# Kernel optimization log

Hardware: AMD Instinct MI355X
Metric: run time of the kernel (lower is better)

## Reference

```python
import jax, jax.numpy as jnp
import numpy as np

B = 32; H = 56; W = 56; C = 384; WS = 7; SHIFT = 3; NH = 12; HID = 1536; RANK = 192
N = WS * WS
NWIN = (H // WS) * (W // WS)


def _rel_index():
    coords = np.stack(np.meshgrid(np.arange(WS), np.arange(WS), indexing='ij')).reshape(2, -1)
    rel = (coords[:, :, None] - coords[:, None, :]).transpose(1, 2, 0)
    rel[..., 0] += WS - 1
    rel[..., 1] += WS - 1
    rel[..., 0] *= 2 * WS - 1
    return jnp.asarray(rel.sum(-1).reshape(-1))  # (N*N,) int


def _attn_mask():
    img = np.zeros((H, W))
    cnt = 0
    sls = (slice(0, -WS), slice(-WS, -SHIFT), slice(-SHIFT, None))
    for hs in sls:
        for ws_ in sls:
            img[hs, ws_] = cnt
            cnt += 1
    mw = img.reshape(H // WS, WS, W // WS, WS).transpose(0, 2, 1, 3).reshape(-1, N)
    am = mw[:, None, :] - mw[:, :, None]
    return jnp.asarray(np.where(am != 0, -100.0, 0.0).astype(np.float32))  # (nW,N,N)


REL_IDX = _rel_index()
ATTN_MASK = _attn_mask()


def _ln(x, g, b):
    m = x.mean(-1, keepdims=True)
    v = ((x - m) ** 2).mean(-1, keepdims=True)
    return (x - m) / jnp.sqrt(v + 1e-5) * g + b


def _flin(x, v, u, b):
    # FactorizedLinear: x @ V^T @ U^T + b
    return (x @ v.T) @ u.T + b


def setup_inputs() -> dict:
    key = jax.random.key(0)
    ks = jax.random.split(key, 12)
    def n(k, shape, s):
        return jax.random.normal(k, shape, jnp.float32) * s
    return {
        'x': jax.random.normal(ks[0], (B, H * W, C), jnp.float32),
        'norm1_g': jnp.ones((C,), jnp.float32), 'norm1_b': jnp.zeros((C,), jnp.float32),
        'rpb_table': n(ks[1], ((2 * WS - 1) ** 2, NH), 0.02),
        'qkv_v': n(ks[2], (RANK, C), 0.05), 'qkv_u': n(ks[3], (3 * C, RANK), 0.05),
        'qkv_b': jnp.zeros((3 * C,), jnp.float32),
        'proj_v': n(ks[4], (RANK, C), 0.05), 'proj_u': n(ks[5], (C, RANK), 0.05),
        'proj_b': jnp.zeros((C,), jnp.float32),
        'norm2_g': jnp.ones((C,), jnp.float32), 'norm2_b': jnp.zeros((C,), jnp.float32),
        'fc1_v': n(ks[6], (RANK, C), 0.05), 'fc1_u': n(ks[7], (HID, RANK), 0.05),
        'fc1_b': jnp.zeros((HID,), jnp.float32),
        'fc2_v': n(ks[8], (RANK, HID), 0.05), 'fc2_u': n(ks[9], (C, RANK), 0.05),
        'fc2_b': jnp.zeros((C,), jnp.float32),
    }


def reference(x, norm1_g, norm1_b, rpb_table, qkv_v, qkv_u, qkv_b,
              proj_v, proj_u, proj_b, norm2_g, norm2_b,
              fc1_v, fc1_u, fc1_b, fc2_v, fc2_u, fc2_b):
    hd = C // NH
    scale = hd ** -0.5
    shortcut = x
    y = _ln(x, norm1_g, norm1_b).reshape(B, H, W, C)
    y = jnp.roll(y, (-SHIFT, -SHIFT), axis=(1, 2))  # cyclic shift
    # window partition -> (B*nW, N, C)
    y = y.reshape(B, H // WS, WS, W // WS, WS, C).transpose(0, 1, 3, 2, 4, 5).reshape(-1, N, C)
    qkv = _flin(y, qkv_v, qkv_u, qkv_b).reshape(-1, N, 3, NH, hd).transpose(2, 0, 3, 1, 4)
    q, k, v = qkv[0] * scale, qkv[1], qkv[2]  # (B*nW, NH, N, hd)
    attn = jnp.einsum('bhnd,bhmd->bhnm', q, k)
    rpb = rpb_table[REL_IDX].reshape(N, N, NH).transpose(2, 0, 1)  # (NH,N,N)
    attn = attn + rpb[None]
    attn = attn.reshape(B, NWIN, NH, N, N) + ATTN_MASK[None, :, None]
    attn = jax.nn.softmax(attn, axis=-1).reshape(-1, NH, N, N)
    o = jnp.einsum('bhnm,bhmd->bhnd', attn, v).transpose(0, 2, 1, 3).reshape(-1, N, C)
    o = _flin(o, proj_v, proj_u, proj_b)
    # window reverse + reverse shift
    o = o.reshape(B, H // WS, W // WS, WS, WS, C).transpose(0, 1, 3, 2, 4, 5).reshape(B, H, W, C)
    o = jnp.roll(o, (SHIFT, SHIFT), axis=(1, 2)).reshape(B, H * W, C)
    x = shortcut + o
    z = _ln(x, norm2_g, norm2_b)
    z = jax.nn.gelu(_flin(z, fc1_v, fc1_u, fc1_b), approximate=False)
    z = _flin(z, fc2_v, fc2_u, fc2_b)
    return x + z
```

## Files before the change

### kernel.cpp

```cpp
#include <hip/hip_runtime.h>
#include <hip/hip_bf16.h>

using bf16 = __hip_bfloat16;
typedef __bf16 bf16x8 __attribute__((ext_vector_type(8)));
typedef __bf16 bf16x4v __attribute__((ext_vector_type(4)));
typedef float f32x4 __attribute__((ext_vector_type(4)));

#define MROWS 100352

__device__ __forceinline__ void async16(void* l, const void* g) {
    void* gg = const_cast<void*>(g);
    __builtin_amdgcn_global_load_lds((__attribute__((address_space(1))) void*)gg,
                                     (__attribute__((address_space(3))) void*)l, 16, 0, 0);
}

__device__ __forceinline__ float gelu_f(float x) {
    float u = x * fmaf(0.044715f * x, x, 1.0f);
    float e = __expf(-1.5957691216057308f * u);
    return x * __builtin_amdgcn_rcpf(1.0f + e);
}

struct Cvt8 { const float* s[8]; bf16* d[8]; int n[8]; };

__global__ __launch_bounds__(256) void cvt8_k(Cvt8 c) {
    int seg = blockIdx.y;
    int i4 = (blockIdx.x * 256 + threadIdx.x) * 4;
    if (i4 < c.n[seg]) {
        float4 v = *(const float4*)(c.s[seg] + i4);
        bf16* d = c.d[seg] + i4;
        d[0] = __float2bfloat16(v.x);
        d[1] = __float2bfloat16(v.y);
        d[2] = __float2bfloat16(v.z);
        d[3] = __float2bfloat16(v.w);
    }
}

__global__ __launch_bounds__(384) void wmerge_k(const float* __restrict__ u,
                                                const float* __restrict__ v,
                                                bf16* __restrict__ wm) {
    int o = blockIdx.x, i = threadIdx.x;
    const float* ur = u + o * 192;
    float acc = 0.f;
    for (int r = 0; r < 192; ++r) acc = fmaf(ur[r], v[r * 384 + i], acc);
    wm[o * 384 + i] = __float2bfloat16(acc);
}

__global__ __launch_bounds__(256) void bias_pre_k(const float* __restrict__ rpbt,
                                                  float* __restrict__ biasf) {
    int wt = blockIdx.x / 12, h = blockIdx.x % 12;
    int t = threadIdx.x;
    int lane = t >> 2, tb = t & 3;
    int hi = lane >> 4, lo = lane & 15;
    int m = tb * 16 + lo;
    bool bH = (wt & 2) != 0, bW = (wt & 1) != 0;
    float* outb = biasf + (size_t)blockIdx.x * 4096;
    int mm = m < 49 ? m : 0;
    int i2 = mm / 7, j2 = mm % 7;
    int rm = (bH ? (i2 < 4 ? 1 : 2) : 0) * 3 + (bW ? (j2 < 4 ? 1 : 2) : 0);
#pragma unroll
    for (int ta = 0; ta < 4; ++ta) {
#pragma unroll
        for (int j = 0; j < 4; ++j) {
            int n = ta * 16 + hi * 4 + j;
            float v;
            if (n < 49 && m < 49) {
                int i1 = n / 7, j1 = n % 7;
                int rn = (bH ? (i1 < 4 ? 1 : 2) : 0) * 3 + (bW ? (j1 < 4 ? 1 : 2) : 0);
                v = rpbt[((i1 - i2 + 6) * 13 + (j1 - j2 + 6)) * 12 + h];
                if (rn != rm) v -= 100.0f;
            } else {
                v = -1e30f;
            }
            outb[(ta * 4 + j) * 256 + t] = v;
        }
    }
}

__global__ __launch_bounds__(256) void ln1_window_k(const float* __restrict__ x,
                                                    const float* __restrict__ g,
                                                    const float* __restrict__ bta,
                                                    bf16* __restrict__ ywin) {
    int wrow = blockIdx.x * 4 + (threadIdx.x >> 6);
    int lane = threadIdx.x & 63;
    int tok = wrow % 49, win = wrow / 49;
    int i = tok / 7, j = tok % 7;
    int wwi = win & 7, whi = (win >> 3) & 7, bi = win >> 6;
    int hs = (whi * 7 + i + 3) % 56;
    int ws_ = (wwi * 7 + j + 3) % 56;
    const float* xr = x + ((size_t)bi * 3136 + (size_t)hs * 56 + ws_) * 384;
    float v[6]; float s = 0.f, s2 = 0.f;
#pragma unroll
    for (int u = 0; u < 6; ++u) { float t = xr[lane + 64 * u]; v[u] = t; s += t; s2 += t * t; }
#pragma unroll
    for (int d = 1; d < 64; d <<= 1) { s += __shfl_xor(s, d); s2 += __shfl_xor(s2, d); }
    float mean = s * (1.0f / 384.0f);
    float var = s2 * (1.0f / 384.0f) - mean * mean;
    float rstd = rsqrtf(var + 1e-5f);
    bf16* yr = ywin + (size_t)wrow * 384;
#pragma unroll
    for (int u = 0; u < 6; ++u) {
        int c = lane + 64 * u;
        yr[c] = __float2bfloat16((v[u] - mean) * rstd * g[c] + bta[c]);
    }
}

__global__ __launch_bounds__(256) void resid_ln2_k(const float* __restrict__ x,
                                                   const bf16* __restrict__ proj,
                                                   const float* __restrict__ g,
                                                   const float* __restrict__ bta,
                                                   float* __restrict__ x2,
                                                   bf16* __restrict__ z) {
    int row = blockIdx.x * 4 + (threadIdx.x >> 6);
    int lane = threadIdx.x & 63;
    int bi = row / 3136; int hw = row % 3136;
    int h = hw / 56, w = hw % 56;
    int h2 = (h + 53) % 56, w2 = (w + 53) % 56;
    int prow = ((bi * 8 + h2 / 7) * 8 + w2 / 7) * 49 + (h2 % 7) * 7 + (w2 % 7);
    const float* xr = x + (size_t)row * 384;
    const bf16* pr = proj + (size_t)prow * 384;
    float* x2r = x2 + (size_t)row * 384;
    float v[6]; float s = 0.f, s2 = 0.f;
#pragma unroll
    for (int u = 0; u < 6; ++u) {
        int c = lane + 64 * u;
        float t = xr[c] + __bfloat162float(pr[c]);
        v[u] = t; s += t; s2 += t * t;
        x2r[c] = t;
    }
#pragma unroll
    for (int d = 1; d < 64; d <<= 1) { s += __shfl_xor(s, d); s2 += __shfl_xor(s2, d); }
    float mean = s * (1.0f / 384.0f);
    float var = s2 * (1.0f / 384.0f) - mean * mean;
    float rstd = rsqrtf(var + 1e-5f);
    bf16* zr = z + (size_t)row * 384;
#pragma unroll
    for (int u = 0; u < 6; ++u) {
        int c = lane + 64 * u;
        zr[c] = __float2bfloat16((v[u] - mean) * rstd * g[c] + bta[c]);
    }
}

__global__ __launch_bounds__(256) void attn_mfma_k(const bf16* __restrict__ qkv,
                                                   const float* __restrict__ biasf,
                                                   bf16* __restrict__ o) {
    __shared__ __align__(16) __bf16 vt_s[4][32 * 72];
    __shared__ __align__(16) __bf16 p_s[4][32 * 72];
    const int win = blockIdx.x;
    const int r = blockIdx.y;
    const int wave = threadIdx.x >> 6, lane = threadIdx.x & 63;
    const int lo = lane & 15, hi = lane >> 4;
    const int whi = (win >> 3) & 7, wwi = win & 7;
    const int wt = ((whi == 7) ? 2 : 0) + ((wwi == 7) ? 1 : 0);
    __bf16* vt_w = vt_s[wave];
    __bf16* p_w = p_s[wave];
    const int h = r * 4 + wave;
    const bf16* qbase = qkv + (size_t)win * 49 * 1152 + h * 32;
    const float* btile = biasf + (size_t)(wt * 12 + h) * 4096;
    bf16x8 zf = {};

    {
        int m = lane;
        bf16x8 vrow[4];
#pragma unroll
        for (int d8 = 0; d8 < 4; ++d8)
            vrow[d8] = (m < 49) ? *(const bf16x8*)(qbase + (size_t)m * 1152 + 768 + d8 * 8) : zf;
#pragma unroll
        for (int d8 = 0; d8 < 4; ++d8)
#pragma unroll
            for (int e = 0; e < 8; ++e)
                vt_w[(d8 * 8 + e) * 72 + m] = vrow[d8][e];
    }
    bf16x8 aq[4], bk[4];
    const int kq = hi * 8;
#pragma unroll
    for (int ta = 0; ta < 4; ++ta) {
        int n = ta * 16 + lo;
        aq[ta] = (n < 49) ? *(const bf16x8*)(qbase + (size_t)n * 1152 + kq) : zf;
        bk[ta] = (n < 49) ? *(const bf16x8*)(qbase + (size_t)n * 1152 + 384 + kq) : zf;
    }
    f32x4 acc[4][4] = {};
#pragma unroll
    for (int ta = 0; ta < 4; ++ta)
#pragma unroll
        for (int tb = 0; tb < 4; ++tb)
            acc[ta][tb] = __builtin_amdgcn_mfma_f32_16x16x32_bf16(aq[ta], bk[tb], acc[ta][tb], 0, 0, 0);
#pragma unroll
    for (int ta = 0; ta < 4; ++ta) {
#pragma unroll
        for (int j = 0; j < 4; ++j) {
            float4 b4 = *(const float4*)(btile + (ta * 4 + j) * 256 + lane * 4);
            acc[ta][0][j] = fmaf(acc[ta][0][j], 0.17677669529663687f, b4.x);
            acc[ta][1][j] = fmaf(acc[ta][1][j], 0.17677669529663687f, b4.y);
            acc[ta][2][j] = fmaf(acc[ta][2][j], 0.17677669529663687f, b4.z);
            acc[ta][3][j] = fmaf(acc[ta][3][j], 0.17677669529663687f, b4.w);
        }
    }
    bf16x8 vb[2][2];
#pragma unroll
    for (int kb = 0; kb < 2; ++kb)
#pragma unroll
        for (int tb = 0; tb < 2; ++tb)
            vb[kb][tb] = *(const bf16x8*)(vt_w + (tb * 16 + lo) * 72 + kb * 32 + hi * 8);

    f32x4 oacc[4][2] = {};
#pragma unroll
    for (int half = 0; half < 2; ++half) {
#pragma unroll
        for (int tq = 0; tq < 2; ++tq) {
            int ta = half * 2 + tq;
#pragma unroll
            for (int j = 0; j < 4; ++j) {
                float mx = fmaxf(fmaxf(acc[ta][0][j], acc[ta][1][j]),
                                 fmaxf(acc[ta][2][j], acc[ta][3][j]));
                mx = fmaxf(mx, __shfl_xor(mx, 1));
                mx = fmaxf(mx, __shfl_xor(mx, 2));
                mx = fmaxf(mx, __shfl_xor(mx, 4));
                mx = fmaxf(mx, __shfl_xor(mx, 8));
                float e0 = __expf(acc[ta][0][j] - mx);
                float e1 = __expf(acc[ta][1][j] - mx);
                float e2 = __expf(acc[ta][2][j] - mx);
                float e3 = __expf(acc[ta][3][j] - mx);
                float sm = e0 + e1 + e2 + e3;
                sm += __shfl_xor(sm, 1);
                sm += __shfl_xor(sm, 2);
                sm += __shfl_xor(sm, 4);
                sm += __shfl_xor(sm, 8);
                float inv = __builtin_amdgcn_rcpf(sm);
                int nl = tq * 16 + hi * 4 + j;
                p_w[nl * 72 + lo]      = (__bf16)(e0 * inv);
                p_w[nl * 72 + 16 + lo] = (__bf16)(e1 * inv);
                p_w[nl * 72 + 32 + lo] = (__bf16)(e2 * inv);
                p_w[nl * 72 + 48 + lo] = (__bf16)(e3 * inv);
            }
        }
#pragma unroll
        for (int kb = 0; kb < 2; ++kb) {
#pragma unroll
            for (int tq = 0; tq < 2; ++tq) {
                bf16x8 pa = *(const bf16x8*)(p_w + (tq * 16 + lo) * 72 + kb * 32 + hi * 8);
#pragma unroll
                for (int tb = 0; tb < 2; ++tb)
                    oacc[half * 2 + tq][tb] =
                        __builtin_amdgcn_mfma_f32_16x16x32_bf16(pa, vb[kb][tb], oacc[half * 2 + tq][tb], 0, 0, 0);
            }
        }
    }
    bf16* obase = o + (size_t)win * 49 * 384 + h * 32;
#pragma unroll
    for (int ta = 0; ta < 4; ++ta) {
#pragma unroll
        for (int j = 0; j < 4; ++j) {
            int n = ta * 16 + hi * 4 + j;
            if (n < 49) {
#pragma unroll
                for (int tb = 0; tb < 2; ++tb)
                    obase[(size_t)n * 384 + tb * 16 + lo] = __float2bfloat16(oacc[ta][tb][j]);
            }
        }
    }
}

template <int K, int N, int WN, int EPI>
__global__ __launch_bounds__(WN * 128, 8 - WN) void gemm_bt(const bf16* __restrict__ A,
                                                            const bf16* __restrict__ W,
                                                            const float* __restrict__ bias,
                                                            void* __restrict__ Cout) {
    constexpr int T = WN * 128;
    constexpr int BN = WN * 32;
    __shared__ __align__(16) bf16 lds_a[128 * 64];
    __shared__ __align__(16) bf16 lds_b[BN * 64];
    const int t = threadIdx.x;
    const int wave = t >> 6, lane = t & 63;
    const int gdx = gridDim.x;
    int flat = blockIdx.y * gdx + blockIdx.x;
    int q = (gdx * gridDim.y) >> 3;
    int work = (flat & 7) * q + (flat >> 3);
    const int n0 = (work % gdx) * BN, m0 = (work / gdx) * 128;
    const int wm = wave / WN, wn = wave % WN;
    const int fr = lane & 15, hi = lane >> 4;
    const int srow = t >> 3;
    const int gslot = (t & 7) ^ (srow & 7);
    const bf16* abase = A + (size_t)(m0 + srow) * K + gslot * 8;
    const bf16* bbase = W + (size_t)(n0 + srow) * K + gslot * 8;
    char* la = (char*)lds_a + t * 16;
    char* lb = (char*)lds_b + t * 16;
    const int fp = fr & 7;
    const char* ra0 = (const char*)lds_a + (wm * 64 + fr) * 128 + (hi ^ fp) * 16;
    const char* ra1 = (const char*)lds_a + (wm * 64 + fr) * 128 + ((4 + hi) ^ fp) * 16;
    const char* rb0 = (const char*)lds_b + (wn * 32 + fr) * 128 + (hi ^ fp) * 16;
    const char* rb1 = (const char*)lds_b + (wn * 32 + fr) * 128 + ((4 + hi) ^ fp) * 16;
    f32x4 acc[4][2] = {};
#pragma unroll
    for (int kt = 0; kt < K; kt += 64) {
        if (kt > 0) __syncthreads();
#pragma unroll
        for (int i = 0; i < 1024 / T; ++i)
            async16(la + i * T * 16, abase + (size_t)i * (T >> 3) * K + kt);
#pragma unroll
        for (int i = 0; i < BN * 8 / T; ++i)
            async16(lb + i * T * 16, bbase + (size_t)i * (T >> 3) * K + kt);
        __syncthreads();
        bf16x8 af[4], bfr[2];
#pragma unroll
        for (int mi = 0; mi < 4; ++mi) af[mi] = *(const bf16x8*)(ra0 + mi * 2048);
#pragma unroll
        for (int ni = 0; ni < 2; ++ni) bfr[ni] = *(const bf16x8*)(rb0 + ni * 2048);
#pragma unroll
        for (int mi = 0; mi < 4; ++mi)
#pragma unroll
            for (int ni = 0; ni < 2; ++ni)
                acc[mi][ni] = __builtin_amdgcn_mfma_f32_16x16x32_bf16(bfr[ni], af[mi], acc[mi][ni], 0, 0, 0);
#pragma unroll
        for (int mi = 0; mi < 4; ++mi) af[mi] = *(const bf16x8*)(ra1 + mi * 2048);
#pragma unroll
        for (int ni = 0; ni < 2; ++ni) bfr[ni] = *(const bf16x8*)(rb1 + ni * 2048);
#pragma unroll
        for (int mi = 0; mi < 4; ++mi)
#pragma unroll
            for (int ni = 0; ni < 2; ++ni)
                acc[mi][ni] = __builtin_amdgcn_mfma_f32_16x16x32_bf16(bfr[ni], af[mi], acc[mi][ni], 0, 0, 0);
    }
    const int rq4 = hi * 4;
    const int ncol = n0 + wn * 32 + rq4;
    const size_t cbase = (size_t)(m0 + wm * 64 + fr) * N + ncol;
    const float* pb = bias ? bias + ncol : nullptr;
#pragma unroll
    for (int mi = 0; mi < 4; ++mi) {
#pragma unroll
        for (int ni = 0; ni < 2; ++ni) {
            float v0 = acc[mi][ni][0], v1 = acc[mi][ni][1];
            float v2 = acc[mi][ni][2], v3 = acc[mi][ni][3];
            if (pb) {
                float4 b4 = *(const float4*)(pb + ni * 16);
                v0 += b4.x; v1 += b4.y; v2 += b4.z; v3 += b4.w;
            }
            if (EPI == 1) { v0 = gelu_f(v0); v1 = gelu_f(v1); v2 = gelu_f(v2); v3 = gelu_f(v3); }
            if (EPI == 2) {
                float4* p = (float4*)((float*)Cout + cbase + (size_t)mi * 16 * N + ni * 16);
                float4 o = *p;
                o.x += v0; o.y += v1; o.z += v2; o.w += v3;
                *p = o;
            } else {
                bf16x4v st = { (__bf16)v0, (__bf16)v1, (__bf16)v2, (__bf16)v3 };
                *(bf16x4v*)((bf16*)Cout + cbase + (size_t)mi * 16 * N + ni * 16) = st;
            }
        }
    }
}

__global__ __launch_bounds__(256, 4) void mlp_mid_k(const bf16* __restrict__ A,
                                                    const bf16* __restrict__ U,
                                                    const bf16* __restrict__ V2,
                                                    const float* __restrict__ b1,
                                                    bf16* __restrict__ Cout) {
    __shared__ __align__(16) bf16 lds_a[64 * 192];
    __shared__ __align__(16) bf16 lds_h[64 * 128];
    const int t = threadIdx.x;
    const int wave = t >> 6, lane = t & 63;
    const int wn = wave;
    const int fr = lane & 15, hi = lane >> 4;
    const int fp = fr & 7;
    const int m0 = blockIdx.x * 64;
#pragma unroll
    for (int i = 0; i < 6; ++i) {
        int u = i * 256 + t;
        int row = u / 24, slot = u % 24;
        int gslot = slot ^ (row & 7);
        async16((char*)lds_a + u * 16, A + (size_t)(m0 + row) * 192 + gslot * 8);
    }
    __syncthreads();

    f32x4 acc2[4][3] = {};
    const bf16* ub = U + (size_t)(wn * 32 + fr) * 192 + hi * 8;
    const bf16* vb = V2 + (size_t)(wn * 48 + fr) * 1536 + hi * 8;

    for (int hc = 0; hc < 12; ++hc) {
        f32x4 acc1[4][2] = {};
#pragma unroll
        for (int kk = 0; kk < 6; ++kk) {
            bf16x8 af[4], bu[2];
#pragma unroll
            for (int mi = 0; mi < 4; ++mi) {
                int row = mi * 16 + fr;
                af[mi] = *(const bf16x8*)((const char*)lds_a + row * 384 + ((kk * 4 + hi) ^ fp) * 16);
            }
#pragma unroll
            for (int nn = 0; nn < 2; ++nn)
                bu[nn] = *(const bf16x8*)(ub + (size_t)(hc * 128 + nn * 16) * 192 + kk * 32);
#pragma unroll
            for (int mi = 0; mi < 4; ++mi)
#pragma unroll
                for (int nn = 0; nn < 2; ++nn)
                    acc1[mi][nn] = __builtin_amdgcn_mfma_f32_16x16x32_bf16(bu[nn], af[mi], acc1[mi][nn], 0, 0, 0);
        }
        if (hc > 0) __syncthreads();
#pragma unroll
        for (int nn = 0; nn < 2; ++nn) {
            float4 b4 = *(const float4*)(b1 + hc * 128 + wn * 32 + nn * 16 + hi * 4);
#pragma unroll
            for (int mi = 0; mi < 4; ++mi) {
                int mrow = mi * 16 + fr;
                float v0 = gelu_f(acc1[mi][nn][0] + b4.x);
                float v1 = gelu_f(acc1[mi][nn][1] + b4.y);
                float v2 = gelu_f(acc1[mi][nn][2] + b4.z);
                float v3 = gelu_f(acc1[mi][nn][3] + b4.w);
                bf16x4v st = { (__bf16)v0, (__bf16)v1, (__bf16)v2, (__bf16)v3 };
                int hb = (wn * 64 + nn * 32 + hi * 8) ^ ((mrow & 7) << 4);
                *(bf16x4v*)((char*)lds_h + mrow * 256 + hb) = st;
            }
        }
        __syncthreads();
#pragma unroll
        for (int kk = 0; kk < 4; ++kk) {
            bf16x8 af2[4], bv[3];
#pragma unroll
            for (int mi = 0; mi < 4; ++mi) {
                int mrow = mi * 16 + fr;
                int kb = (kk * 64 + hi * 16) ^ ((mrow & 7) << 4);
                af2[mi] = *(const bf16x8*)((const char*)lds_h + mrow * 256 + kb);
            }
#pragma unroll
            for (int tn = 0; tn < 3; ++tn)
                bv[tn] = *(const bf16x8*)(vb + (size_t)(tn * 16) * 1536 + hc * 128 + kk * 32);
#pragma unroll
            for (int mi = 0; mi < 4; ++mi)
#pragma unroll
                for (int tn = 0; tn < 3; ++tn)
                    acc2[mi][tn] = __builtin_amdgcn_mfma_f32_16x16x32_bf16(bv[tn], af2[mi], acc2[mi][tn], 0, 0, 0);
        }
    }
    const size_t cbase = (size_t)(m0 + fr) * 192 + wn * 48 + hi * 4;
#pragma unroll
    for (int mi = 0; mi < 4; ++mi) {
#pragma unroll
        for (int tn = 0; tn < 3; ++tn) {
            bf16x4v st = { (__bf16)acc2[mi][tn][0], (__bf16)acc2[mi][tn][1],
                           (__bf16)acc2[mi][tn][2], (__bf16)acc2[mi][tn][3] };
            *(bf16x4v*)(Cout + cbase + (size_t)mi * 16 * 192 + tn * 16) = st;
        }
    }
}

extern "C" void kernel_launch(void* const* d_in, const int* in_sizes, int n_in,
                              void* d_out, int out_size, void* d_ws, size_t ws_size,
                              hipStream_t stream) {
    const float* x      = (const float*)d_in[0];
    const float* n1g    = (const float*)d_in[1];
    const float* n1b    = (const float*)d_in[2];
    const float* rpbt   = (const float*)d_in[3];
    const float* qkv_v  = (const float*)d_in[4];
    const float* qkv_u  = (const float*)d_in[5];
    const float* qkv_b  = (const float*)d_in[6];
    const float* proj_v = (const float*)d_in[7];
    const float* proj_u = (const float*)d_in[8];
    const float* proj_b = (const float*)d_in[9];
    const float* n2g    = (const float*)d_in[10];
    const float* n2b    = (const float*)d_in[11];
    const float* fc1_v  = (const float*)d_in[12];
    const float* fc1_u  = (const float*)d_in[13];
    const float* fc1_b  = (const float*)d_in[14];
    const float* fc2_v  = (const float*)d_in[15];
    const float* fc2_u  = (const float*)d_in[16];
    const float* fc2_b  = (const float*)d_in[17];

    char* ws = (char*)d_ws;
    bf16* wb = (bf16*)ws;
    bf16* w_qkv_v  = wb;
    bf16* w_qkv_u  = wb + 73728;
    bf16* w_proj_v = wb + 294912;
    bf16* w_proj_u = wb + 368640;
    bf16* w_fc1_v  = wb + 442368;
    bf16* w_fc1_u  = wb + 516096;
    bf16* w_fc2_v  = wb + 811008;
    bf16* w_fc2_u  = wb + 1105920;
    bf16* w_proj_m = wb + 1179648;
    float* biasf   = (float*)(ws + 3145728);
    size_t off = (size_t)4 << 20;
    bf16* R1 = (bf16*)(ws + off); off += (size_t)MROWS * 1536 * 2;
    bf16* R2 = (bf16*)(ws + off); off += (size_t)MROWS * 384 * 2;
    bf16* R3 = (bf16*)(ws + off);
    float* out = (float*)d_out;

    Cvt8 c;
    c.s[0] = qkv_v;  c.d[0] = w_qkv_v;  c.n[0] = 73728;
    c.s[1] = qkv_u;  c.d[1] = w_qkv_u;  c.n[1] = 221184;
    c.s[2] = proj_v; c.d[2] = w_proj_v; c.n[2] = 73728;
    c.s[3] = proj_u; c.d[3] = w_proj_u; c.n[3] = 73728;
    c.s[4] = fc1_v;  c.d[4] = w_fc1_v;  c.n[4] = 73728;
    c.s[5] = fc1_u;  c.d[5] = w_fc1_u;  c.n[5] = 294912;
    c.s[6] = fc2_v;  c.d[6] = w_fc2_v;  c.n[6] = 294912;
    c.s[7] = fc2_u;  c.d[7] = w_fc2_u;  c.n[7] = 73728;
    cvt8_k<<<dim3(288, 8), 256, 0, stream>>>(c);
    bias_pre_k<<<48, 256, 0, stream>>>(rpbt, biasf);
    wmerge_k<<<384, 384, 0, stream>>>(proj_u, proj_v, w_proj_m);

    ln1_window_k<<<MROWS / 4, 256, 0, stream>>>(x, n1g, n1b, R2);
    gemm_bt<384, 192, 2, 0><<<dim3(3, 784), 256, 0, stream>>>(R2, w_qkv_v, nullptr, R3);
    gemm_bt<192, 1152, 4, 0><<<dim3(9, 784), 512, 0, stream>>>(R3, w_qkv_u, qkv_b, R1);
    attn_mfma_k<<<dim3(2048, 3), 256, 0, stream>>>(R1, biasf, R2);
    gemm_bt<384, 384, 4, 0><<<dim3(3, 784), 512, 0, stream>>>(R2, w_proj_m, proj_b, R1);
    resid_ln2_k<<<MROWS / 4, 256, 0, stream>>>(x, R1, n2g, n2b, out, R2);
    gemm_bt<384, 192, 2, 0><<<dim3(3, 784), 256, 0, stream>>>(R2, w_fc1_v, nullptr, R3);
    mlp_mid_k<<<1568, 256, 0, stream>>>(R3, w_fc1_u, w_fc2_v, fc1_b, R1);
    gemm_bt<192, 384, 4, 2><<<dim3(3, 784), 512, 0, stream>>>(R1, w_fc2_u, fc2_b, out);
}
```

Before: 810.7 us.

## Double-buffer hidden tile in fused MLP kernel and prefetch U weights into registers

```diff
diff --git a/kernel.cpp b/kernel.cpp
--- a/kernel.cpp
+++ b/kernel.cpp
@@ -348,13 +348,13 @@
     }
 }
 
-__global__ __launch_bounds__(256, 4) void mlp_mid_k(const bf16* __restrict__ A,
+__global__ __launch_bounds__(256, 3) void mlp_mid_k(const bf16* __restrict__ A,
                                                     const bf16* __restrict__ U,
                                                     const bf16* __restrict__ V2,
                                                     const float* __restrict__ b1,
                                                     bf16* __restrict__ Cout) {
     __shared__ __align__(16) bf16 lds_a[64 * 192];
-    __shared__ __align__(16) bf16 lds_h[64 * 128];
+    __shared__ __align__(16) bf16 lds_h[2][64 * 72];
     const int t = threadIdx.x;
     const int wave = t >> 6, lane = t & 63;
     const int wn = wave;
@@ -368,66 +368,76 @@
         int gslot = slot ^ (row & 7);
         async16((char*)lds_a + u * 16, A + (size_t)(m0 + row) * 192 + gslot * 8);
     }
+
+    const bf16* ub = U + (size_t)(wn * 16 + fr) * 192 + hi * 8;
+    const bf16* vb = V2 + (size_t)(wn * 48 + fr) * 1536 + hi * 8;
+    bf16x8 buc[6], bun[6];
+#pragma unroll
+    for (int kk = 0; kk < 6; ++kk)
+        buc[kk] = *(const bf16x8*)(ub + kk * 32);
     __syncthreads();
 
     f32x4 acc2[4][3] = {};
-    const bf16* ub = U + (size_t)(wn * 32 + fr) * 192 + hi * 8;
-    const bf16* vb = V2 + (size_t)(wn * 48 + fr) * 1536 + hi * 8;
-
-    for (int hc = 0; hc < 12; ++hc) {
-        f32x4 acc1[4][2] = {};
+#pragma unroll 1
+    for (int hc = 0; hc < 24; ++hc) {
+        bf16x8 bvc[2][3];
+#pragma unroll
+        for (int kk2 = 0; kk2 < 2; ++kk2)
+#pragma unroll
+            for (int tn = 0; tn < 3; ++tn)
+                bvc[kk2][tn] = *(const bf16x8*)(vb + (size_t)(tn * 16) * 1536 + hc * 64 + kk2 * 32);
+        if (hc + 1 < 24) {
+#pragma unroll
+            for (int kk = 0; kk < 6; ++kk)
+                bun[kk] = *(const bf16x8*)(ub + (size_t)(hc + 1) * 64 * 192 + kk * 32);
+        }
+        f32x4 acc1[4] = {};
 #pragma unroll
         for (int kk = 0; kk < 6; ++kk) {
-            bf16x8 af[4], bu[2];
+            bf16x8 af[4];
 #pragma unroll
             for (int mi = 0; mi < 4; ++mi) {
                 int row = mi * 16 + fr;
                 af[mi] = *(const bf16x8*)((const char*)lds_a + row * 384 + ((kk * 4 + hi) ^ fp) * 16);
             }
 #pragma unroll
-            for (int nn = 0; nn < 2; ++nn)
-                bu[nn] = *(const bf16x8*)(ub + (size_t)(hc * 128 + nn * 16) * 192 + kk * 32);
-#pragma unroll
             for (int mi = 0; mi < 4; ++mi)
-#pragma unroll
-                for (int nn = 0; nn < 2; ++nn)
-                    acc1[mi][nn] = __builtin_amdgcn_mfma_f32_16x16x32_bf16(bu[nn], af[mi], acc1[mi][nn], 0, 0, 0);
-        }
-        if (hc > 0) __syncthreads();
-#pragma unroll
-        for (int nn = 0; nn < 2; ++nn) {
-            float4 b4 = *(const float4*)(b1 + hc * 128 + wn * 32 + nn * 16 + hi * 4);
+                acc1[mi] = __builtin_amdgcn_mfma_f32_16x16x32_bf16(buc[kk], af[mi], acc1[mi], 0, 0, 0);
+        }
+        {
+            bf16* hbuf = lds_h[hc & 1];
+            float4 b4 = *(const float4*)(b1 + hc * 64 + wn * 16 + hi * 4);
 #pragma unroll
             for (int mi = 0; mi < 4; ++mi) {
                 int mrow = mi * 16 + fr;
-                float v0 = gelu_f(acc1[mi][nn][0] + b4.x);
-                float v1 = gelu_f(acc1[mi][nn][1] + b4.y);
-                float v2 = gelu_f(acc1[mi][nn][2] + b4.z);
-                float v3 = gelu_f(acc1[mi][nn][3] + b4.w);
+                float v0 = gelu_f(acc1[mi][0] + b4.x);
+                float v1 = gelu_f(acc1[mi][1] + b4.y);
+                float v2 = gelu_f(acc1[mi][2] + b4.z);
+                float v3 = gelu_f(acc1[mi][3] + b4.w);
                 bf16x4v st = { (__bf16)v0, (__bf16)v1, (__bf16)v2, (__bf16)v3 };
-                int hb = (wn * 64 + nn * 32 + hi * 8) ^ ((mrow & 7) << 4);
-                *(bf16x4v*)((char*)lds_h + mrow * 256 + hb) = st;
+                *(bf16x4v*)(hbuf + mrow * 72 + wn * 16 + hi * 4) = st;
             }
         }
         __syncthreads();
-#pragma unroll
-        for (int kk = 0; kk < 4; ++kk) {
-            bf16x8 af2[4], bv[3];
-#pragma unroll
-            for (int mi = 0; mi < 4; ++mi) {
-                int mrow = mi * 16 + fr;
-                int kb = (kk * 64 + hi * 16) ^ ((mrow & 7) << 4);
-                af2[mi] = *(const bf16x8*)((const char*)lds_h + mrow * 256 + kb);
-            }
-#pragma unroll
-            for (int tn = 0; tn < 3; ++tn)
-                bv[tn] = *(const bf16x8*)(vb + (size_t)(tn * 16) * 1536 + hc * 128 + kk * 32);
-#pragma unroll
-            for (int mi = 0; mi < 4; ++mi)
-#pragma unroll
-                for (int tn = 0; tn < 3; ++tn)
-                    acc2[mi][tn] = __builtin_amdgcn_mfma_f32_16x16x32_bf16(bv[tn], af2[mi], acc2[mi][tn], 0, 0, 0);
-        }
+        {
+            const bf16* hbuf = lds_h[hc & 1];
+#pragma unroll
+            for (int kk2 = 0; kk2 < 2; ++kk2) {
+                bf16x8 af2[4];
+#pragma unroll
+                for (int mi = 0; mi < 4; ++mi) {
+                    int mrow = mi * 16 + fr;
+                    af2[mi] = *(const bf16x8*)(hbuf + mrow * 72 + kk2 * 32 + hi * 8);
+                }
+#pragma unroll
+                for (int mi = 0; mi < 4; ++mi)
+#pragma unroll
+                    for (int tn = 0; tn < 3; ++tn)
+                        acc2[mi][tn] = __builtin_amdgcn_mfma_f32_16x16x32_bf16(bvc[kk2][tn], af2[mi], acc2[mi][tn], 0, 0, 0);
+            }
+        }
+#pragma unroll
+        for (int kk = 0; kk < 6; ++kk) buc[kk] = bun[kk];
     }
     const size_t cbase = (size_t)(m0 + fr) * 192 + wn * 48 + hi * 4;
 #pragma unroll
```

Result: no change. 810.1 us (-0.1%).
